# Optimization experiments

Measured on AMD Instinct MI355X. Metric: run time of the kernel, lower is better.

## Reference

```python
import jax, jax.numpy as jnp
import numpy as np

B, L = 4, 1024
D_MODEL, D_STATE, N_LAYERS, EXPAND = 512, 16, 4, 2
ED = EXPAND * D_MODEL            # 1024
DT_RANK = -(-D_MODEL // 16)       # ceil(d_model/16) = 32
D_CONV = 4
N_IN, N_OUT, N_FUT = 3, 2, 10
EPS = 1e-5


def setup_inputs() -> dict:
    key = jax.random.key(0)
    ks = jax.random.split(key, 16)
    s = 0.05
    inp = {
        "temporal_seq": jax.random.normal(ks[0], (B, L, N_IN), jnp.float32),
        # input / output projections (torch Linear: weight [out,in])
        "Wi": jax.random.normal(ks[1], (D_MODEL, N_IN), jnp.float32) * s,
        "bi": jnp.zeros((D_MODEL,), jnp.float32),
        "Wo": jax.random.normal(ks[2], (N_FUT * N_OUT, D_MODEL), jnp.float32) * s,
        "bo": jnp.zeros((N_FUT * N_OUT,), jnp.float32),
        # final LayerNorm
        "ln_g": jnp.ones((D_MODEL,), jnp.float32),
        "ln_b": jnp.zeros((D_MODEL,), jnp.float32),
        # stacked per-layer MambaBlock params
        "lWin": jax.random.normal(ks[3], (N_LAYERS, 2 * ED, D_MODEL), jnp.float32) * s,
        "lconvw": jax.random.normal(ks[4], (N_LAYERS, ED, 1, D_CONV), jnp.float32) * 0.2,
        "lconvb": jnp.zeros((N_LAYERS, ED), jnp.float32),
        "lWx": jax.random.normal(ks[5], (N_LAYERS, DT_RANK + 2 * D_STATE, ED), jnp.float32) * s,
        "lWdt": jax.random.normal(ks[6], (N_LAYERS, ED, DT_RANK), jnp.float32) * s,
        "lbdt": jnp.full((N_LAYERS, ED), -3.0, jnp.float32),  # small initial dt
        "lAlog": jnp.log(jnp.broadcast_to(jnp.arange(1.0, D_STATE + 1.0, dtype=jnp.float32), (N_LAYERS, ED, D_STATE))),
        "lD": jnp.ones((N_LAYERS, ED), jnp.float32),
        "lWout": jax.random.normal(ks[7], (N_LAYERS, D_MODEL, ED), jnp.float32) * s,
    }
    return inp


def _scan_op(l, r):
    al, bl = l
    ar, br = r
    return al * ar, ar * bl + br


def _mamba_block(x, Win, convw, convb, Wx, Wdt, bdt, Alog, Dp, Wout):
    # x: [B, L, D_MODEL]
    xz = jnp.einsum("bld,ed->ble", x, Win)          # [B, L, 2*ED]
    xb, z = jnp.split(xz, 2, axis=-1)
    # causal depthwise conv1d (padding d_conv-1 on the left == torch pad+trim)
    xc = jnp.transpose(xb, (0, 2, 1))                 # [B, ED, L]
    xc = jax.lax.conv_general_dilated(xc, convw, (1,), [(D_CONV - 1, 0)], feature_group_count=ED)
    xb = jnp.transpose(xc + convb[None, :, None], (0, 2, 1))
    xb = jax.nn.silu(xb)                              # [B, L, ED]
    # SSM parameters
    dbc = jnp.einsum("ble,fe->blf", xb, Wx)          # [B, L, DT_RANK+2N]
    delta = jax.nn.softplus(dbc[..., :DT_RANK] @ Wdt.T + bdt)   # [B, L, ED]
    Bm = dbc[..., DT_RANK:DT_RANK + D_STATE]          # [B, L, N]
    Cm = dbc[..., DT_RANK + D_STATE:]                 # [B, L, N]
    A = -jnp.exp(Alog)                                # [ED, N]
    dA = jnp.exp(delta[..., None] * A)                # [B, L, ED, N]
    dBx = (delta * xb)[..., None] * Bm[:, :, None, :] # [B, L, ED, N]
    # parallel associative scan: h_t = dA_t * h_{t-1} + dBx_t
    _, hs = jax.lax.associative_scan(_scan_op, (dA, dBx), axis=1)
    y = jnp.einsum("blen,bln->ble", hs, Cm) + Dp * xb
    y = y * jax.nn.silu(z)
    return jnp.einsum("ble,de->bld", y, Wout)


def reference(temporal_seq, Wi, bi, Wo, bo, ln_g, ln_b, lWin, lconvw, lconvb, lWx, lWdt, lbdt, lAlog, lD, lWout):
    x = temporal_seq @ Wi.T + bi                      # [B, L, D_MODEL]
    for i in range(N_LAYERS):
        x = _mamba_block(x, lWin[i], lconvw[i], lconvb[i], lWx[i], lWdt[i], lbdt[i], lAlog[i], lD[i], lWout[i])
    mu = jnp.mean(x, axis=-1, keepdims=True)
    var = jnp.mean((x - mu) ** 2, axis=-1, keepdims=True)
    x = (x - mu) / jnp.sqrt(var + EPS) * ln_g + ln_b
    h_final = x[:, -1, :]                             # [B, D_MODEL]
    u = h_final @ Wo.T + bo                           # [B, N_FUT*N_OUT]
    return u.reshape(-1, N_FUT, N_OUT)
```

## Files before the change

### kernel.cpp

```cpp
#include <hip/hip_runtime.h>
#include <hip/hip_bf16.h>
#include <math.h>

constexpr int Bx = 4, Lx = 1024, DM = 512, DS = 16, NL = 4, EDx = 1024;
constexpr int DTR = 32;

typedef __attribute__((ext_vector_type(8))) short short8v;
typedef __attribute__((ext_vector_type(4))) float f32x4;

__device__ inline short f2bf(float f) {
  union { __hip_bfloat16 h; short s; } u;
  u.h = __float2bfloat16(f);
  return u.s;
}
__device__ inline float bf2f(short s) {
  union { __hip_bfloat16 h; short s; } u;
  u.s = s;
  return __bfloat162float(u.h);
}

__global__ __launch_bounds__(256) void k_init_x(const float* __restrict__ seq,
    const float* __restrict__ Wi, const float* __restrict__ bi, float* __restrict__ x) {
  int idx = blockIdx.x * 256 + threadIdx.x;
  int d = idx & (DM - 1);
  int bl = idx >> 9;
  float s0 = seq[bl * 3 + 0], s1 = seq[bl * 3 + 1], s2 = seq[bl * 3 + 2];
  x[idx] = bi[d] + s0 * Wi[d * 3 + 0] + s1 * Wi[d * 3 + 1] + s2 * Wi[d * 3 + 2];
}

template <int BM, int BN>
__global__ __launch_bounds__(256) void k_gemm_mfma(
    const float* __restrict__ A, int lda,
    const float* __restrict__ W, int ldw,
    float* __restrict__ C, int ldc, int K) {
  constexpr int MR = BM / 32, NR = BN / 32;
  __shared__ short Ah[BM][44], Al[BM][44], Bh[BN][44], Bl[BN][44];
  const int tid = threadIdx.x;
  const int w = tid >> 6, lane = tid & 63;
  const int wr = w >> 1, wc = w & 1;
  const int r16 = lane & 15, kh = lane >> 4;
  const int m0 = blockIdx.x * BM, n0 = blockIdx.y * BN;

  f32x4 acc[MR][NR];
  #pragma unroll
  for (int i = 0; i < MR; ++i)
    #pragma unroll
    for (int j = 0; j < NR; ++j) {
      acc[i][j][0] = 0.f; acc[i][j][1] = 0.f; acc[i][j][2] = 0.f; acc[i][j][3] = 0.f;
    }

  for (int k0 = 0; k0 < K; k0 += 32) {
    __syncthreads();
    #pragma unroll
    for (int p = 0; p < BM / 32; ++p) {
      int f = tid + p * 256;
      int r = f >> 3, c = (f & 7) << 2;
      const float4 v = *(const float4*)(A + (size_t)(m0 + r) * lda + k0 + c);
      short h0 = f2bf(v.x), h1 = f2bf(v.y), h2 = f2bf(v.z), h3 = f2bf(v.w);
      Ah[r][c + 0] = h0; Ah[r][c + 1] = h1; Ah[r][c + 2] = h2; Ah[r][c + 3] = h3;
      Al[r][c + 0] = f2bf(v.x - bf2f(h0));
      Al[r][c + 1] = f2bf(v.y - bf2f(h1));
      Al[r][c + 2] = f2bf(v.z - bf2f(h2));
      Al[r][c + 3] = f2bf(v.w - bf2f(h3));
    }
    #pragma unroll
    for (int p = 0; p < BN / 32; ++p) {
      int f = tid + p * 256;
      int r = f >> 3, c = (f & 7) << 2;
      const float4 v = *(const float4*)(W + (size_t)(n0 + r) * ldw + k0 + c);
      short h0 = f2bf(v.x), h1 = f2bf(v.y), h2 = f2bf(v.z), h3 = f2bf(v.w);
      Bh[r][c + 0] = h0; Bh[r][c + 1] = h1; Bh[r][c + 2] = h2; Bh[r][c + 3] = h3;
      Bl[r][c + 0] = f2bf(v.x - bf2f(h0));
      Bl[r][c + 1] = f2bf(v.y - bf2f(h1));
      Bl[r][c + 2] = f2bf(v.z - bf2f(h2));
      Bl[r][c + 3] = f2bf(v.w - bf2f(h3));
    }
    __syncthreads();
    short8v ah[MR], al[MR], bh[NR], bl[NR];
    #pragma unroll
    for (int i = 0; i < MR; ++i) {
      int rr = wr * (BM / 2) + i * 16 + r16;
      ah[i] = *(const short8v*)(&Ah[rr][kh * 8]);
      al[i] = *(const short8v*)(&Al[rr][kh * 8]);
    }
    #pragma unroll
    for (int j = 0; j < NR; ++j) {
      int cc = wc * (BN / 2) + j * 16 + r16;
      bh[j] = *(const short8v*)(&Bh[cc][kh * 8]);
      bl[j] = *(const short8v*)(&Bl[cc][kh * 8]);
    }
    #pragma unroll
    for (int i = 0; i < MR; ++i)
      #pragma unroll
      for (int j = 0; j < NR; ++j) {
        acc[i][j] = __builtin_amdgcn_mfma_f32_16x16x32_bf16(ah[i], bh[j], acc[i][j], 0, 0, 0);
        acc[i][j] = __builtin_amdgcn_mfma_f32_16x16x32_bf16(ah[i], bl[j], acc[i][j], 0, 0, 0);
        acc[i][j] = __builtin_amdgcn_mfma_f32_16x16x32_bf16(al[i], bh[j], acc[i][j], 0, 0, 0);
      }
  }
  #pragma unroll
  for (int i = 0; i < MR; ++i) {
    int row_base = m0 + wr * (BM / 2) + i * 16 + kh * 4;
    #pragma unroll
    for (int j = 0; j < NR; ++j) {
      int col = n0 + wc * (BN / 2) + j * 16 + r16;
      #pragma unroll
      for (int r = 0; r < 4; ++r)
        C[(size_t)(row_base + r) * ldc + col] = acc[i][j][r];
    }
  }
}

template <int SK>
__global__ __launch_bounds__(256) void k_xproj_mfma(
    const float* __restrict__ A,
    const float* __restrict__ W,
    float* __restrict__ PART) {
  constexpr int BM = 128, BN = 64, KS = 1024 / SK;
  constexpr int MR = 4, NR = 2;
  __shared__ short Ah[BM][44], Al[BM][44], Bh[BN][44], Bl[BN][44];
  const int tid = threadIdx.x;
  const int w = tid >> 6, lane = tid & 63;
  const int wr = w >> 1, wc = w & 1;
  const int r16 = lane & 15, kh = lane >> 4;
  const int m0 = blockIdx.x * BM;
  const int kbeg = blockIdx.z * KS;

  f32x4 acc[MR][NR];
  #pragma unroll
  for (int i = 0; i < MR; ++i)
    #pragma unroll
    for (int j = 0; j < NR; ++j) {
      acc[i][j][0] = 0.f; acc[i][j][1] = 0.f; acc[i][j][2] = 0.f; acc[i][j][3] = 0.f;
    }

  for (int k0 = kbeg; k0 < kbeg + KS; k0 += 32) {
    __syncthreads();
    #pragma unroll
    for (int p = 0; p < BM / 32; ++p) {
      int f = tid + p * 256;
      int r = f >> 3, c = (f & 7) << 2;
      const float4 v = *(const float4*)(A + (size_t)(m0 + r) * 1024 + k0 + c);
      short h0 = f2bf(v.x), h1 = f2bf(v.y), h2 = f2bf(v.z), h3 = f2bf(v.w);
      Ah[r][c + 0] = h0; Ah[r][c + 1] = h1; Ah[r][c + 2] = h2; Ah[r][c + 3] = h3;
      Al[r][c + 0] = f2bf(v.x - bf2f(h0));
      Al[r][c + 1] = f2bf(v.y - bf2f(h1));
      Al[r][c + 2] = f2bf(v.z - bf2f(h2));
      Al[r][c + 3] = f2bf(v.w - bf2f(h3));
    }
    #pragma unroll
    for (int p = 0; p < BN / 32; ++p) {
      int f = tid + p * 256;
      int r = f >> 3, c = (f & 7) << 2;
      const float4 v = *(const float4*)(W + (size_t)r * 1024 + k0 + c);
      short h0 = f2bf(v.x), h1 = f2bf(v.y), h2 = f2bf(v.z), h3 = f2bf(v.w);
      Bh[r][c + 0] = h0; Bh[r][c + 1] = h1; Bh[r][c + 2] = h2; Bh[r][c + 3] = h3;
      Bl[r][c + 0] = f2bf(v.x - bf2f(h0));
      Bl[r][c + 1] = f2bf(v.y - bf2f(h1));
      Bl[r][c + 2] = f2bf(v.z - bf2f(h2));
      Bl[r][c + 3] = f2bf(v.w - bf2f(h3));
    }
    __syncthreads();
    short8v ah[MR], al[MR], bh[NR], bl[NR];
    #pragma unroll
    for (int i = 0; i < MR; ++i) {
      int rr = wr * 64 + i * 16 + r16;
      ah[i] = *(const short8v*)(&Ah[rr][kh * 8]);
      al[i] = *(const short8v*)(&Al[rr][kh * 8]);
    }
    #pragma unroll
    for (int j = 0; j < NR; ++j) {
      int cc = wc * 32 + j * 16 + r16;
      bh[j] = *(const short8v*)(&Bh[cc][kh * 8]);
      bl[j] = *(const short8v*)(&Bl[cc][kh * 8]);
    }
    #pragma unroll
    for (int i = 0; i < MR; ++i)
      #pragma unroll
      for (int j = 0; j < NR; ++j) {
        acc[i][j] = __builtin_amdgcn_mfma_f32_16x16x32_bf16(ah[i], bh[j], acc[i][j], 0, 0, 0);
        acc[i][j] = __builtin_amdgcn_mfma_f32_16x16x32_bf16(ah[i], bl[j], acc[i][j], 0, 0, 0);
        acc[i][j] = __builtin_amdgcn_mfma_f32_16x16x32_bf16(al[i], bh[j], acc[i][j], 0, 0, 0);
      }
  }
  float* Cp = PART + (size_t)blockIdx.z * (4096 * 64);
  #pragma unroll
  for (int i = 0; i < MR; ++i) {
    int row_base = m0 + wr * 64 + i * 16 + kh * 4;
    #pragma unroll
    for (int j = 0; j < NR; ++j) {
      int col = wc * 32 + j * 16 + r16;
      #pragma unroll
      for (int r = 0; r < 4; ++r)
        Cp[(size_t)(row_base + r) * 64 + col] = acc[i][j][r];
    }
  }
}

template <int SK>
__global__ __launch_bounds__(256) void k_redux(const float* __restrict__ PART,
                                               float* __restrict__ out) {
  int i = blockIdx.x * 256 + threadIdx.x;
  float4 s = ((const float4*)PART)[i];
  #pragma unroll
  for (int k = 1; k < SK; ++k) {
    const float4 v = ((const float4*)PART)[i + k * 65536];
    s.x += v.x; s.y += v.y; s.z += v.z; s.w += v.w;
  }
  ((float4*)out)[i] = s;
}

template <int BM, int BN, int EPI>
__global__ __launch_bounds__(256) void k_gemm_tn(
    const float* __restrict__ A, int lda,
    const float* __restrict__ W, int ldw,
    const float* __restrict__ bias,
    float* __restrict__ C, int ldc, int K) {
  constexpr int BK = 16;
  constexpr int MR = BM / 16, NR = BN / 16;
  __shared__ float As[BK][BM + 4];
  __shared__ float Bs[BK][BN + 4];
  const int tid = threadIdx.x;
  const int tx = tid & 15, ty = tid >> 4;
  const int m0 = blockIdx.x * BM, n0 = blockIdx.y * BN;
  const int arow = tid >> 2;
  const int akol = (tid & 3) << 2;
  float acc[MR][NR] = {};
  for (int k0 = 0; k0 < K; k0 += BK) {
    #pragma unroll
    for (int r = 0; r < BM / 64; ++r) {
      int m = arow + r * 64;
      const float4 v = *(const float4*)(A + (size_t)(m0 + m) * lda + k0 + akol);
      As[akol + 0][m] = v.x; As[akol + 1][m] = v.y;
      As[akol + 2][m] = v.z; As[akol + 3][m] = v.w;
    }
    if constexpr (BN >= 64) {
      #pragma unroll
      for (int r = 0; r < BN / 64; ++r) {
        int n = arow + r * 64;
        const float4 v = *(const float4*)(W + (size_t)(n0 + n) * ldw + k0 + akol);
        Bs[akol + 0][n] = v.x; Bs[akol + 1][n] = v.y;
        Bs[akol + 2][n] = v.z; Bs[akol + 3][n] = v.w;
      }
    } else {
      if (arow < BN) {
        const float4 v = *(const float4*)(W + (size_t)(n0 + arow) * ldw + k0 + akol);
        Bs[akol + 0][arow] = v.x; Bs[akol + 1][arow] = v.y;
        Bs[akol + 2][arow] = v.z; Bs[akol + 3][arow] = v.w;
      }
    }
    __syncthreads();
    #pragma unroll
    for (int k = 0; k < BK; ++k) {
      float af[MR], bf[NR];
      #pragma unroll
      for (int i = 0; i < MR; ++i) af[i] = As[k][ty * MR + i];
      #pragma unroll
      for (int j = 0; j < NR; ++j) bf[j] = Bs[k][tx * NR + j];
      #pragma unroll
      for (int i = 0; i < MR; ++i)
        #pragma unroll
        for (int j = 0; j < NR; ++j)
          acc[i][j] = fmaf(af[i], bf[j], acc[i][j]);
    }
    __syncthreads();
  }
  #pragma unroll
  for (int i = 0; i < MR; ++i) {
    int m = m0 + ty * MR + i;
    #pragma unroll
    for (int j = 0; j < NR; ++j) {
      int n = n0 + tx * NR + j;
      float v = acc[i][j];
      if constexpr (EPI == 1) {
        v += bias[n];
        v = (v > 20.f) ? v : log1pf(__expf(v));
      }
      C[(size_t)m * ldc + n] = v;
    }
  }
}

__global__ __launch_bounds__(256) void k_conv_silu(const float* __restrict__ xz,
    const float* __restrict__ cw, const float* __restrict__ cb, float* __restrict__ xb) {
  int idx = blockIdx.x * 256 + threadIdx.x;
  int e = idx & (EDx - 1);
  int bl = idx >> 10;
  int l = bl & (Lx - 1);
  const float4 w = ((const float4*)cw)[e];
  float acc = cb[e];
  if (l - 3 >= 0) acc = fmaf(xz[(size_t)(bl - 3) * (2 * EDx) + e], w.x, acc);
  if (l - 2 >= 0) acc = fmaf(xz[(size_t)(bl - 2) * (2 * EDx) + e], w.y, acc);
  if (l - 1 >= 0) acc = fmaf(xz[(size_t)(bl - 1) * (2 * EDx) + e], w.z, acc);
  acc = fmaf(xz[(size_t)bl * (2 * EDx) + e], w.w, acc);
  xb[idx] = acc / (1.f + __expf(-acc));
}

#define CVT4(V) { V.x = -__expf(V.x) * 1.44269504f; V.y = -__expf(V.y) * 1.44269504f; \
                  V.z = -__expf(V.z) * 1.44269504f; V.w = -__expf(V.w) * 1.44269504f; }

#define ST4PQ(Av, Pv, Qv, Bv) { \
  float a0 = exp2f(dl * Av.x); Pv.x *= a0; Qv.x = fmaf(a0, Qv.x, dx * Bv.x); \
  float a1 = exp2f(dl * Av.y); Pv.y *= a1; Qv.y = fmaf(a1, Qv.y, dx * Bv.y); \
  float a2 = exp2f(dl * Av.z); Pv.z *= a2; Qv.z = fmaf(a2, Qv.z, dx * Bv.z); \
  float a3 = exp2f(dl * Av.w); Pv.w *= a3; Qv.w = fmaf(a3, Qv.w, dx * Bv.w); }

#define ST4Y(Av, Hv, Bv, Cv) { \
  float a0 = exp2f(dl * Av.x); Hv.x = fmaf(a0, Hv.x, dx * Bv.x); y = fmaf(Hv.x, Cv.x, y); \
  float a1 = exp2f(dl * Av.y); Hv.y = fmaf(a1, Hv.y, dx * Bv.y); y = fmaf(Hv.y, Cv.y, y); \
  float a2 = exp2f(dl * Av.z); Hv.z = fmaf(a2, Hv.z, dx * Bv.z); y = fmaf(Hv.z, Cv.z, y); \
  float a3 = exp2f(dl * Av.w); Hv.w = fmaf(a3, Hv.w, dx * Bv.w); y = fmaf(Hv.w, Cv.w, y); }

template <int NCt>
__global__ __launch_bounds__(256) void k_scan1(
    const float* __restrict__ del, const float* __restrict__ xb,
    const float* __restrict__ dbc, const float* __restrict__ Alog,
    float* __restrict__ PQ) {
  constexpr int CTt = Lx / NCt;
  const int idx = blockIdx.x * 256 + threadIdx.x;
  const int ch = idx & 4095, c = idx >> 12;
  const int b = ch >> 10, e = ch & 1023;
  float4 A0, A1, A2, A3;
  {
    const float4* ar = (const float4*)(Alog + e * DS);
    A0 = ar[0]; A1 = ar[1]; A2 = ar[2]; A3 = ar[3];
    CVT4(A0); CVT4(A1); CVT4(A2); CVT4(A3);
  }
  float4 P0 = {1,1,1,1}, P1 = {1,1,1,1}, P2 = {1,1,1,1}, P3 = {1,1,1,1};
  float4 Q0 = {0,0,0,0}, Q1 = {0,0,0,0}, Q2 = {0,0,0,0}, Q3 = {0,0,0,0};
  const size_t bl0 = (size_t)b * Lx + c * CTt;
  const float* dp  = del + bl0 * EDx + e;
  const float* xp  = xb  + bl0 * EDx + e;
  const float* bcp = dbc + bl0 * 64 + 32;
  #pragma unroll 2
  for (int i = 0; i < CTt; ++i) {
    float dl = dp[0];
    float xbl = xp[0];
    float dx = dl * xbl;
    const float4* bp = (const float4*)bcp;
    float4 B0 = bp[0], B1 = bp[1], B2 = bp[2], B3 = bp[3];
    ST4PQ(A0, P0, Q0, B0); ST4PQ(A1, P1, Q1, B1);
    ST4PQ(A2, P2, Q2, B2); ST4PQ(A3, P3, Q3, B3);
    dp += EDx; xp += EDx; bcp += 64;
  }
  float4* o = (float4*)(PQ + (size_t)idx * 32);
  o[0] = P0; o[1] = P1; o[2] = P2; o[3] = P3;
  o[4] = Q0; o[5] = Q1; o[6] = Q2; o[7] = Q3;
}

template <int NCt>
__global__ __launch_bounds__(256) void k_scan2(float* __restrict__ PQ) {
  const int idx = blockIdx.x * 256 + threadIdx.x;
  const int ch = idx >> 4, n = idx & 15;
  constexpr int G = 8;
  const size_t off = (size_t)ch * 32 + n;
  float Pa[G], Qa[G], Pb[G], Qb[G];
  #pragma unroll
  for (int j = 0; j < G; ++j) {
    size_t base = (size_t)j * (4096 * 32) + off;
    Pa[j] = PQ[base]; Qa[j] = PQ[base + 16];
  }
  float H = 0.f;
  #pragma unroll
  for (int gp = 0; gp < NCt / (2 * G); ++gp) {
    const int cA = 2 * gp * G, cB = (2 * gp + 1) * G, cN = (2 * gp + 2) * G;
    #pragma unroll
    for (int j = 0; j < G; ++j) {
      size_t base = (size_t)(cB + j) * (4096 * 32) + off;
      Pb[j] = PQ[base]; Qb[j] = PQ[base + 16];
    }
    #pragma unroll
    for (int j = 0; j < G; ++j) {
      size_t base = (size_t)(cA + j) * (4096 * 32) + off;
      PQ[base + 16] = H;
      H = fmaf(Pa[j], H, Qa[j]);
    }
    if (gp + 1 < NCt / (2 * G)) {
      #pragma unroll
      for (int j = 0; j < G; ++j) {
        size_t base = (size_t)(cN + j) * (4096 * 32) + off;
        Pa[j] = PQ[base]; Qa[j] = PQ[base + 16];
      }
    }
    #pragma unroll
    for (int j = 0; j < G; ++j) {
      size_t base = (size_t)(cB + j) * (4096 * 32) + off;
      PQ[base + 16] = H;
      H = fmaf(Pb[j], H, Qb[j]);
    }
  }
}

template <int NCt>
__global__ __launch_bounds__(256) void k_scan3(
    float* __restrict__ dy,
    const float* __restrict__ xb,
    const float* __restrict__ dbc,
    const float* __restrict__ xz,
    const float* __restrict__ Alog, const float* __restrict__ Dp,
    const float* __restrict__ PQ) {
  constexpr int CTt = Lx / NCt;
  const int idx = blockIdx.x * 256 + threadIdx.x;
  const int ch = idx & 4095, c = idx >> 12;
  const int b = ch >> 10, e = ch & 1023;
  float4 A0, A1, A2, A3;
  {
    const float4* ar = (const float4*)(Alog + e * DS);
    A0 = ar[0]; A1 = ar[1]; A2 = ar[2]; A3 = ar[3];
    CVT4(A0); CVT4(A1); CVT4(A2); CVT4(A3);
  }
  float4 H0, H1, H2, H3;
  {
    const float4* hi = (const float4*)(PQ + (size_t)idx * 32 + 16);
    H0 = hi[0]; H1 = hi[1]; H2 = hi[2]; H3 = hi[3];
  }
  const float De = Dp[e];
  const size_t bl0 = (size_t)b * Lx + c * CTt;
  float* dyp = dy + bl0 * EDx + e;
  const float* xp  = xb + bl0 * EDx + e;
  const float* bcp = dbc + bl0 * 64 + 32;
  const float* zp  = xz + bl0 * (2 * EDx) + EDx + e;
  #pragma unroll 2
  for (int i = 0; i < CTt; ++i) {
    float dl = dyp[0];
    float xbl = xp[0];
    float zv = zp[0];
    float dx = dl * xbl;
    const float4* bp = (const float4*)bcp;
    float4 B0 = bp[0], B1 = bp[1], B2 = bp[2], B3 = bp[3];
    float4 C0 = bp[4], C1 = bp[5], C2 = bp[6], C3 = bp[7];
    float y = 0.f;
    ST4Y(A0, H0, B0, C0); ST4Y(A1, H1, B1, C1);
    ST4Y(A2, H2, B2, C2); ST4Y(A3, H3, B3, C3);
    y = fmaf(De, xbl, y);
    y *= zv / (1.f + __expf(-zv));
    dyp[0] = y;
    dyp += EDx; xp += EDx; bcp += 64; zp += 2 * EDx;
  }
}

__global__ __launch_bounds__(256) void k_ln_head(
    const float* __restrict__ x, const float* __restrict__ g,
    const float* __restrict__ be, const float* __restrict__ Wo,
    const float* __restrict__ bo, float* __restrict__ out) {
  const int b = blockIdx.x;
  const int t = threadIdx.x;
  const float* xr = x + ((size_t)b * Lx + (Lx - 1)) * DM;
  __shared__ float w1[4], w2[4];
  __shared__ float xn[DM];
  __shared__ float hp[20][8];
  float a0 = xr[t], a1 = xr[t + 256];
  float p = a0 + a1;
  #pragma unroll
  for (int o = 32; o > 0; o >>= 1) p += __shfl_down(p, o);
  if ((t & 63) == 0) w1[t >> 6] = p;
  __syncthreads();
  float mean = (w1[0] + w1[1] + w1[2] + w1[3]) * (1.f / DM);
  float d0 = a0 - mean, d1 = a1 - mean;
  p = d0 * d0 + d1 * d1;
  #pragma unroll
  for (int o = 32; o > 0; o >>= 1) p += __shfl_down(p, o);
  if ((t & 63) == 0) w2[t >> 6] = p;
  __syncthreads();
  float rstd = rsqrtf((w2[0] + w2[1] + w2[2] + w2[3]) * (1.f / DM) + 1e-5f);
  xn[t] = d0 * rstd * g[t] + be[t];
  xn[t + 256] = d1 * rstd * g[t + 256] + be[t + 256];
  __syncthreads();
  if (t < 160) {
    int j = t / 8, sg = t % 8;
    const float* wr = Wo + (size_t)j * DM + sg * 64;
    const float* xs = xn + sg * 64;
    float s = 0.f;
    #pragma unroll
    for (int k = 0; k < 64; ++k) s = fmaf(xs[k], wr[k], s);
    hp[j][sg] = s;
  }
  __syncthreads();
  if (t < 20) {
    float s = bo[t];
    #pragma unroll
    for (int k = 0; k < 8; ++k) s += hp[t][k];
    out[b * 20 + t] = s;
  }
}

extern "C" void kernel_launch(void* const* d_in, const int* in_sizes, int n_in,
                              void* d_out, int out_size, void* d_ws, size_t ws_size,
                              hipStream_t stream) {
  (void)in_sizes; (void)n_in; (void)out_size;
  const float* seq    = (const float*)d_in[0];
  const float* Wi     = (const float*)d_in[1];
  const float* bi     = (const float*)d_in[2];
  const float* Wo     = (const float*)d_in[3];
  const float* bo     = (const float*)d_in[4];
  const float* ln_g   = (const float*)d_in[5];
  const float* ln_b   = (const float*)d_in[6];
  const float* lWin   = (const float*)d_in[7];
  const float* lconvw = (const float*)d_in[8];
  const float* lconvb = (const float*)d_in[9];
  const float* lWx    = (const float*)d_in[10];
  const float* lWdt   = (const float*)d_in[11];
  const float* lbdt   = (const float*)d_in[12];
  const float* lAlog  = (const float*)d_in[13];
  const float* lD     = (const float*)d_in[14];
  const float* lWout  = (const float*)d_in[15];

  float* ws  = (float*)d_ws;
  float* X   = ws;
  float* XZ  = X + 2097152;
  float* XB  = XZ + 8388608;
  float* DBC = XB + 4194304;
  float* DEL = DBC + 262144;
  float* PQ  = DEL + 4194304;
  float* PART = PQ;

  const bool big = ws_size >= (size_t)110100480;

  k_init_x<<<dim3(Bx * Lx * DM / 256), 256, 0, stream>>>(seq, Wi, bi, X);

  for (int i = 0; i < NL; ++i) {
    const float* Win  = lWin   + (size_t)i * 2048 * 512;
    const float* cw   = lconvw + (size_t)i * EDx * 4;
    const float* cb   = lconvb + (size_t)i * EDx;
    const float* Wx   = lWx    + (size_t)i * 64 * EDx;
    const float* Wdt  = lWdt   + (size_t)i * EDx * DTR;
    const float* bdt  = lbdt   + (size_t)i * EDx;
    const float* Alog = lAlog  + (size_t)i * EDx * DS;
    const float* Dp   = lD     + (size_t)i * EDx;
    const float* Wout = lWout  + (size_t)i * DM * EDx;

    k_gemm_mfma<128, 128><<<dim3(32, 16), 256, 0, stream>>>(X, DM, Win, DM, XZ, 2 * EDx, DM);
    k_conv_silu<<<dim3(Bx * Lx * EDx / 256), 256, 0, stream>>>(XZ, cw, cb, XB);
    k_xproj_mfma<8><<<dim3(32, 1, 8), 256, 0, stream>>>(XB, Wx, PART);
    k_redux<8><<<dim3(256), 256, 0, stream>>>(PART, DBC);
    k_gemm_tn<128, 64, 1><<<dim3(32, 16), 256, 0, stream>>>(DBC, 64, Wdt, DTR, bdt, DEL, EDx, DTR);
    if (big) {
      k_scan1<64><<<dim3(4096 * 64 / 256), 256, 0, stream>>>(DEL, XB, DBC, Alog, PQ);
      k_scan2<64><<<dim3(4096 * DS / 256), 256, 0, stream>>>(PQ);
      k_scan3<64><<<dim3(4096 * 64 / 256), 256, 0, stream>>>(DEL, XB, DBC, XZ, Alog, Dp, PQ);
    } else {
      k_scan1<32><<<dim3(4096 * 32 / 256), 256, 0, stream>>>(DEL, XB, DBC, Alog, PQ);
      k_scan2<32><<<dim3(4096 * DS / 256), 256, 0, stream>>>(PQ);
      k_scan3<32><<<dim3(4096 * 32 / 256), 256, 0, stream>>>(DEL, XB, DBC, XZ, Alog, Dp, PQ);
    }
    k_gemm_mfma<128, 64><<<dim3(32, 8), 256, 0, stream>>>(DEL, EDx, Wout, EDx, X, DM, EDx);
  }

  k_ln_head<<<dim3(Bx), 256, 0, stream>>>(X, ln_g, ln_b, Wo, bo, (float*)d_out);
}
```

Before: 911.0 us.

## Pre-split GEMM operands into bf16 hi/lo buffers, vectorize conv, raise scan chunks

Adds a k_split kernel that converts fp32 activations and weights into separate bf16 hi/lo arrays before each GEMM. The GEMM then loads pre-split shorts directly instead of converting per tile, which removes repeated conversion work across blocks that reread the same rows. The depthwise conv+SiLU is vectorized to process four channels per thread with float4 loads. The scan chunk count moves from 64 to 128 when the workspace is large enough. The trade-off is extra kernel launches and extra global memory traffic for the split buffers, which are rebuilt every call, including for the weights.

```diff
diff --git a/kernel.cpp b/kernel.cpp
--- a/kernel.cpp
+++ b/kernel.cpp
@@ -6,6 +6,7 @@
 constexpr int DTR = 32;
 
 typedef __attribute__((ext_vector_type(8))) short short8v;
+typedef __attribute__((ext_vector_type(4))) short short4v;
 typedef __attribute__((ext_vector_type(4))) float f32x4;
 
 __device__ inline short f2bf(float f) {
@@ -17,6 +18,10 @@
   union { __hip_bfloat16 h; short s; } u;
   u.s = s;
   return __bfloat162float(u.h);
+}
+__device__ inline void store8(short* p, short8v v) {
+  *(short4v*)(p)     = __builtin_shufflevector(v, v, 0, 1, 2, 3);
+  *(short4v*)(p + 4) = __builtin_shufflevector(v, v, 4, 5, 6, 7);
 }
 
 __global__ __launch_bounds__(256) void k_init_x(const float* __restrict__ seq,
@@ -28,10 +33,23 @@
   x[idx] = bi[d] + s0 * Wi[d * 3 + 0] + s1 * Wi[d * 3 + 1] + s2 * Wi[d * 3 + 2];
 }
 
+__global__ __launch_bounds__(256) void k_split(const float* __restrict__ s,
+    short* __restrict__ hi, short* __restrict__ lo) {
+  int i = blockIdx.x * 256 + threadIdx.x;
+  const float4 v = ((const float4*)s)[i];
+  short4v h, l;
+  h.x = f2bf(v.x); l.x = f2bf(v.x - bf2f(h.x));
+  h.y = f2bf(v.y); l.y = f2bf(v.y - bf2f(h.y));
+  h.z = f2bf(v.z); l.z = f2bf(v.z - bf2f(h.z));
+  h.w = f2bf(v.w); l.w = f2bf(v.w - bf2f(h.w));
+  ((short4v*)hi)[i] = h;
+  ((short4v*)lo)[i] = l;
+}
+
 template <int BM, int BN>
-__global__ __launch_bounds__(256) void k_gemm_mfma(
-    const float* __restrict__ A, int lda,
-    const float* __restrict__ W, int ldw,
+__global__ __launch_bounds__(256) void k_gemm_bfp(
+    const short* __restrict__ Ahg, const short* __restrict__ Alg,
+    const short* __restrict__ Bhg, const short* __restrict__ Blg,
     float* __restrict__ C, int ldc, int K) {
   constexpr int MR = BM / 32, NR = BN / 32;
   __shared__ short Ah[BM][44], Al[BM][44], Bh[BN][44], Bl[BN][44];
@@ -52,28 +70,20 @@
   for (int k0 = 0; k0 < K; k0 += 32) {
     __syncthreads();
     #pragma unroll
-    for (int p = 0; p < BM / 32; ++p) {
+    for (int p = 0; p < BM / 64; ++p) {
       int f = tid + p * 256;
-      int r = f >> 3, c = (f & 7) << 2;
-      const float4 v = *(const float4*)(A + (size_t)(m0 + r) * lda + k0 + c);
-      short h0 = f2bf(v.x), h1 = f2bf(v.y), h2 = f2bf(v.z), h3 = f2bf(v.w);
-      Ah[r][c + 0] = h0; Ah[r][c + 1] = h1; Ah[r][c + 2] = h2; Ah[r][c + 3] = h3;
-      Al[r][c + 0] = f2bf(v.x - bf2f(h0));
-      Al[r][c + 1] = f2bf(v.y - bf2f(h1));
-      Al[r][c + 2] = f2bf(v.z - bf2f(h2));
-      Al[r][c + 3] = f2bf(v.w - bf2f(h3));
-    }
-    #pragma unroll
-    for (int p = 0; p < BN / 32; ++p) {
+      int r = f >> 2, c8 = (f & 3) << 3;
+      size_t g = (size_t)(m0 + r) * K + k0 + c8;
+      store8(&Ah[r][c8], *(const short8v*)(Ahg + g));
+      store8(&Al[r][c8], *(const short8v*)(Alg + g));
+    }
+    #pragma unroll
+    for (int p = 0; p < BN / 64; ++p) {
       int f = tid + p * 256;
-      int r = f >> 3, c = (f & 7) << 2;
-      const float4 v = *(const float4*)(W + (size_t)(n0 + r) * ldw + k0 + c);
-      short h0 = f2bf(v.x), h1 = f2bf(v.y), h2 = f2bf(v.z), h3 = f2bf(v.w);
-      Bh[r][c + 0] = h0; Bh[r][c + 1] = h1; Bh[r][c + 2] = h2; Bh[r][c + 3] = h3;
-      Bl[r][c + 0] = f2bf(v.x - bf2f(h0));
-      Bl[r][c + 1] = f2bf(v.y - bf2f(h1));
-      Bl[r][c + 2] = f2bf(v.z - bf2f(h2));
-      Bl[r][c + 3] = f2bf(v.w - bf2f(h3));
+      int r = f >> 2, c8 = (f & 3) << 3;
+      size_t g = (size_t)(n0 + r) * K + k0 + c8;
+      store8(&Bh[r][c8], *(const short8v*)(Bhg + g));
+      store8(&Bl[r][c8], *(const short8v*)(Blg + g));
     }
     __syncthreads();
     short8v ah[MR], al[MR], bh[NR], bl[NR];
@@ -281,19 +291,35 @@
   }
 }
 
-__global__ __launch_bounds__(256) void k_conv_silu(const float* __restrict__ xz,
+__global__ __launch_bounds__(256) void k_conv_silu4(const float* __restrict__ xz,
     const float* __restrict__ cw, const float* __restrict__ cb, float* __restrict__ xb) {
   int idx = blockIdx.x * 256 + threadIdx.x;
-  int e = idx & (EDx - 1);
-  int bl = idx >> 10;
+  int e4 = (idx & 255) << 2;
+  int bl = idx >> 8;
   int l = bl & (Lx - 1);
-  const float4 w = ((const float4*)cw)[e];
-  float acc = cb[e];
-  if (l - 3 >= 0) acc = fmaf(xz[(size_t)(bl - 3) * (2 * EDx) + e], w.x, acc);
-  if (l - 2 >= 0) acc = fmaf(xz[(size_t)(bl - 2) * (2 * EDx) + e], w.y, acc);
-  if (l - 1 >= 0) acc = fmaf(xz[(size_t)(bl - 1) * (2 * EDx) + e], w.z, acc);
-  acc = fmaf(xz[(size_t)bl * (2 * EDx) + e], w.w, acc);
-  xb[idx] = acc / (1.f + __expf(-acc));
+  const float4 w0 = ((const float4*)cw)[e4 + 0];
+  const float4 w1 = ((const float4*)cw)[e4 + 1];
+  const float4 w2 = ((const float4*)cw)[e4 + 2];
+  const float4 w3 = ((const float4*)cw)[e4 + 3];
+  float4 acc = ((const float4*)cb)[idx & 255];
+  const float* base = xz + (size_t)bl * (2 * EDx) + e4;
+  if (l >= 3) { const float4 x = *(const float4*)(base - 3 * 2 * EDx);
+    acc.x = fmaf(x.x, w0.x, acc.x); acc.y = fmaf(x.y, w1.x, acc.y);
+    acc.z = fmaf(x.z, w2.x, acc.z); acc.w = fmaf(x.w, w3.x, acc.w); }
+  if (l >= 2) { const float4 x = *(const float4*)(base - 2 * 2 * EDx);
+    acc.x = fmaf(x.x, w0.y, acc.x); acc.y = fmaf(x.y, w1.y, acc.y);
+    acc.z = fmaf(x.z, w2.y, acc.z); acc.w = fmaf(x.w, w3.y, acc.w); }
+  if (l >= 1) { const float4 x = *(const float4*)(base - 1 * 2 * EDx);
+    acc.x = fmaf(x.x, w0.z, acc.x); acc.y = fmaf(x.y, w1.z, acc.y);
+    acc.z = fmaf(x.z, w2.z, acc.z); acc.w = fmaf(x.w, w3.z, acc.w); }
+  { const float4 x = *(const float4*)(base);
+    acc.x = fmaf(x.x, w0.w, acc.x); acc.y = fmaf(x.y, w1.w, acc.y);
+    acc.z = fmaf(x.z, w2.w, acc.z); acc.w = fmaf(x.w, w3.w, acc.w); }
+  acc.x /= (1.f + __expf(-acc.x));
+  acc.y /= (1.f + __expf(-acc.y));
+  acc.z /= (1.f + __expf(-acc.z));
+  acc.w /= (1.f + __expf(-acc.w));
+  ((float4*)xb)[idx] = acc;
 }
 
 #define CVT4(V) { V.x = -__expf(V.x) * 1.44269504f; V.y = -__expf(V.y) * 1.44269504f; \
@@ -512,9 +538,19 @@
   float* DBC = XB + 4194304;
   float* DEL = DBC + 262144;
   float* PQ  = DEL + 4194304;
-  float* PART = PQ;
-
-  const bool big = ws_size >= (size_t)110100480;
+
+  short* PQs   = (short*)PQ;
+  short* Xh    = PQs;
+  short* Xl    = PQs + 2097152;
+  short* Winh  = PQs + 4194304;
+  short* Winl  = PQs + 5242880;
+  short* Yh    = PQs;
+  short* Yl    = PQs + 4194304;
+  short* Wouth = PQs + 8388608;
+  short* Woutl = PQs + 8912896;
+  float* PART  = PQ;
+
+  const bool nc128 = ws_size >= (size_t)143654912;
 
   k_init_x<<<dim3(Bx * Lx * DM / 256), 256, 0, stream>>>(seq, Wi, bi, X);
 
@@ -529,21 +565,25 @@
     const float* Dp   = lD     + (size_t)i * EDx;
     const float* Wout = lWout  + (size_t)i * DM * EDx;
 
-    k_gemm_mfma<128, 128><<<dim3(32, 16), 256, 0, stream>>>(X, DM, Win, DM, XZ, 2 * EDx, DM);
-    k_conv_silu<<<dim3(Bx * Lx * EDx / 256), 256, 0, stream>>>(XZ, cw, cb, XB);
+    k_split<<<dim3(2048), 256, 0, stream>>>(X, Xh, Xl);
+    k_split<<<dim3(1024), 256, 0, stream>>>(Win, Winh, Winl);
+    k_gemm_bfp<128, 128><<<dim3(32, 16), 256, 0, stream>>>(Xh, Xl, Winh, Winl, XZ, 2 * EDx, DM);
+    k_conv_silu4<<<dim3(Bx * Lx * EDx / 1024), 256, 0, stream>>>(XZ, cw, cb, XB);
     k_xproj_mfma<8><<<dim3(32, 1, 8), 256, 0, stream>>>(XB, Wx, PART);
     k_redux<8><<<dim3(256), 256, 0, stream>>>(PART, DBC);
     k_gemm_tn<128, 64, 1><<<dim3(32, 16), 256, 0, stream>>>(DBC, 64, Wdt, DTR, bdt, DEL, EDx, DTR);
-    if (big) {
+    if (nc128) {
+      k_scan1<128><<<dim3(4096 * 128 / 256), 256, 0, stream>>>(DEL, XB, DBC, Alog, PQ);
+      k_scan2<128><<<dim3(4096 * DS / 256), 256, 0, stream>>>(PQ);
+      k_scan3<128><<<dim3(4096 * 128 / 256), 256, 0, stream>>>(DEL, XB, DBC, XZ, Alog, Dp, PQ);
+    } else {
       k_scan1<64><<<dim3(4096 * 64 / 256), 256, 0, stream>>>(DEL, XB, DBC, Alog, PQ);
       k_scan2<64><<<dim3(4096 * DS / 256), 256, 0, stream>>>(PQ);
       k_scan3<64><<<dim3(4096 * 64 / 256), 256, 0, stream>>>(DEL, XB, DBC, XZ, Alog, Dp, PQ);
-    } else {
-      k_scan1<32><<<dim3(4096 * 32 / 256), 256, 0, stream>>>(DEL, XB, DBC, Alog, PQ);
-      k_scan2<32><<<dim3(4096 * DS / 256), 256, 0, stream>>>(PQ);
-      k_scan3<32><<<dim3(4096 * 32 / 256), 256, 0, stream>>>(DEL, XB, DBC, XZ, Alog, Dp, PQ);
-    }
-    k_gemm_mfma<128, 64><<<dim3(32, 8), 256, 0, stream>>>(DEL, EDx, Wout, EDx, X, DM, EDx);
+    }
+    k_split<<<dim3(4096), 256, 0, stream>>>(DEL, Yh, Yl);
+    k_split<<<dim3(512), 256, 0, stream>>>(Wout, Wouth, Woutl);
+    k_gemm_bfp<128, 64><<<dim3(32, 8), 256, 0, stream>>>(Yh, Yl, Wouth, Woutl, X, DM, EDx);
   }
 
   k_ln_head<<<dim3(Bx), 256, 0, stream>>>(X, ln_g, ln_b, Wo, bo, (float*)d_out);
```

After: 966.1 us. +6.0%, slower.

## Split scan state across thread pairs and vectorise conv-silu with float4

Applied to the files above, without the earlier changes.

The chunked scan kernels now give each (batch, channel, chunk) to two threads, each holding 8 of the 16 state dims. The pair combines its partial outputs with a lane shuffle and only one lane writes y. This doubles the thread count and halves per-thread registers, to raise occupancy and latency hiding in the scan. The cost is duplicated loads of delta, x and z per pair and an extra shuffle per step. The depthwise conv+SiLU kernel is also rewritten so each thread handles four channels with float4 loads and stores.

```diff
diff --git a/kernel.cpp b/kernel.cpp
--- a/kernel.cpp
+++ b/kernel.cpp
@@ -281,19 +281,35 @@
   }
 }
 
-__global__ __launch_bounds__(256) void k_conv_silu(const float* __restrict__ xz,
+__global__ __launch_bounds__(256) void k_conv_silu4(const float* __restrict__ xz,
     const float* __restrict__ cw, const float* __restrict__ cb, float* __restrict__ xb) {
   int idx = blockIdx.x * 256 + threadIdx.x;
-  int e = idx & (EDx - 1);
-  int bl = idx >> 10;
+  int e4 = (idx & 255) << 2;
+  int bl = idx >> 8;
   int l = bl & (Lx - 1);
-  const float4 w = ((const float4*)cw)[e];
-  float acc = cb[e];
-  if (l - 3 >= 0) acc = fmaf(xz[(size_t)(bl - 3) * (2 * EDx) + e], w.x, acc);
-  if (l - 2 >= 0) acc = fmaf(xz[(size_t)(bl - 2) * (2 * EDx) + e], w.y, acc);
-  if (l - 1 >= 0) acc = fmaf(xz[(size_t)(bl - 1) * (2 * EDx) + e], w.z, acc);
-  acc = fmaf(xz[(size_t)bl * (2 * EDx) + e], w.w, acc);
-  xb[idx] = acc / (1.f + __expf(-acc));
+  const float4 w0 = ((const float4*)cw)[e4 + 0];
+  const float4 w1 = ((const float4*)cw)[e4 + 1];
+  const float4 w2 = ((const float4*)cw)[e4 + 2];
+  const float4 w3 = ((const float4*)cw)[e4 + 3];
+  float4 acc = ((const float4*)cb)[idx & 255];
+  const float* base = xz + (size_t)bl * (2 * EDx) + e4;
+  if (l >= 3) { const float4 x = *(const float4*)(base - 3 * 2 * EDx);
+    acc.x = fmaf(x.x, w0.x, acc.x); acc.y = fmaf(x.y, w1.x, acc.y);
+    acc.z = fmaf(x.z, w2.x, acc.z); acc.w = fmaf(x.w, w3.x, acc.w); }
+  if (l >= 2) { const float4 x = *(const float4*)(base - 2 * 2 * EDx);
+    acc.x = fmaf(x.x, w0.y, acc.x); acc.y = fmaf(x.y, w1.y, acc.y);
+    acc.z = fmaf(x.z, w2.y, acc.z); acc.w = fmaf(x.w, w3.y, acc.w); }
+  if (l >= 1) { const float4 x = *(const float4*)(base - 1 * 2 * EDx);
+    acc.x = fmaf(x.x, w0.z, acc.x); acc.y = fmaf(x.y, w1.z, acc.y);
+    acc.z = fmaf(x.z, w2.z, acc.z); acc.w = fmaf(x.w, w3.z, acc.w); }
+  { const float4 x = *(const float4*)(base);
+    acc.x = fmaf(x.x, w0.w, acc.x); acc.y = fmaf(x.y, w1.w, acc.y);
+    acc.z = fmaf(x.z, w2.w, acc.z); acc.w = fmaf(x.w, w3.w, acc.w); }
+  acc.x /= (1.f + __expf(-acc.x));
+  acc.y /= (1.f + __expf(-acc.y));
+  acc.z /= (1.f + __expf(-acc.z));
+  acc.w /= (1.f + __expf(-acc.w));
+  ((float4*)xb)[idx] = acc;
 }
 
 #define CVT4(V) { V.x = -__expf(V.x) * 1.44269504f; V.y = -__expf(V.y) * 1.44269504f; \
@@ -318,34 +334,35 @@
     float* __restrict__ PQ) {
   constexpr int CTt = Lx / NCt;
   const int idx = blockIdx.x * 256 + threadIdx.x;
-  const int ch = idx & 4095, c = idx >> 12;
+  const int h8 = (idx & 1) << 3;
+  const int g = idx >> 1;
+  const int ch = g & 4095, c = g >> 12;
   const int b = ch >> 10, e = ch & 1023;
-  float4 A0, A1, A2, A3;
+  float4 A0, A1;
   {
-    const float4* ar = (const float4*)(Alog + e * DS);
-    A0 = ar[0]; A1 = ar[1]; A2 = ar[2]; A3 = ar[3];
-    CVT4(A0); CVT4(A1); CVT4(A2); CVT4(A3);
-  }
-  float4 P0 = {1,1,1,1}, P1 = {1,1,1,1}, P2 = {1,1,1,1}, P3 = {1,1,1,1};
-  float4 Q0 = {0,0,0,0}, Q1 = {0,0,0,0}, Q2 = {0,0,0,0}, Q3 = {0,0,0,0};
+    const float4* ar = (const float4*)(Alog + e * DS + h8);
+    A0 = ar[0]; A1 = ar[1];
+    CVT4(A0); CVT4(A1);
+  }
+  float4 P0 = {1,1,1,1}, P1 = {1,1,1,1};
+  float4 Q0 = {0,0,0,0}, Q1 = {0,0,0,0};
   const size_t bl0 = (size_t)b * Lx + c * CTt;
   const float* dp  = del + bl0 * EDx + e;
   const float* xp  = xb  + bl0 * EDx + e;
-  const float* bcp = dbc + bl0 * 64 + 32;
-  #pragma unroll 2
+  const float* bcp = dbc + bl0 * 64 + 32 + h8;
+  #pragma unroll 4
   for (int i = 0; i < CTt; ++i) {
     float dl = dp[0];
     float xbl = xp[0];
     float dx = dl * xbl;
     const float4* bp = (const float4*)bcp;
-    float4 B0 = bp[0], B1 = bp[1], B2 = bp[2], B3 = bp[3];
+    float4 B0 = bp[0], B1 = bp[1];
     ST4PQ(A0, P0, Q0, B0); ST4PQ(A1, P1, Q1, B1);
-    ST4PQ(A2, P2, Q2, B2); ST4PQ(A3, P3, Q3, B3);
     dp += EDx; xp += EDx; bcp += 64;
   }
-  float4* o = (float4*)(PQ + (size_t)idx * 32);
-  o[0] = P0; o[1] = P1; o[2] = P2; o[3] = P3;
-  o[4] = Q0; o[5] = Q1; o[6] = Q2; o[7] = Q3;
+  float4* o = (float4*)(PQ + (size_t)g * 32 + h8);
+  o[0] = P0; o[1] = P1;
+  o[4] = Q0; o[5] = Q1;
 }
 
 template <int NCt>
@@ -401,40 +418,43 @@
     const float* __restrict__ PQ) {
   constexpr int CTt = Lx / NCt;
   const int idx = blockIdx.x * 256 + threadIdx.x;
-  const int ch = idx & 4095, c = idx >> 12;
+  const int hh = idx & 1;
+  const int h8 = hh << 3;
+  const int g = idx >> 1;
+  const int ch = g & 4095, c = g >> 12;
   const int b = ch >> 10, e = ch & 1023;
-  float4 A0, A1, A2, A3;
+  float4 A0, A1;
   {
-    const float4* ar = (const float4*)(Alog + e * DS);
-    A0 = ar[0]; A1 = ar[1]; A2 = ar[2]; A3 = ar[3];
-    CVT4(A0); CVT4(A1); CVT4(A2); CVT4(A3);
-  }
-  float4 H0, H1, H2, H3;
+    const float4* ar = (const float4*)(Alog + e * DS + h8);
+    A0 = ar[0]; A1 = ar[1];
+    CVT4(A0); CVT4(A1);
+  }
+  float4 H0, H1;
   {
-    const float4* hi = (const float4*)(PQ + (size_t)idx * 32 + 16);
-    H0 = hi[0]; H1 = hi[1]; H2 = hi[2]; H3 = hi[3];
+    const float4* hi = (const float4*)(PQ + (size_t)g * 32 + 16 + h8);
+    H0 = hi[0]; H1 = hi[1];
   }
   const float De = Dp[e];
   const size_t bl0 = (size_t)b * Lx + c * CTt;
   float* dyp = dy + bl0 * EDx + e;
   const float* xp  = xb + bl0 * EDx + e;
-  const float* bcp = dbc + bl0 * 64 + 32;
+  const float* bcp = dbc + bl0 * 64 + 32 + h8;
   const float* zp  = xz + bl0 * (2 * EDx) + EDx + e;
-  #pragma unroll 2
+  #pragma unroll 4
   for (int i = 0; i < CTt; ++i) {
     float dl = dyp[0];
     float xbl = xp[0];
     float zv = zp[0];
     float dx = dl * xbl;
     const float4* bp = (const float4*)bcp;
-    float4 B0 = bp[0], B1 = bp[1], B2 = bp[2], B3 = bp[3];
-    float4 C0 = bp[4], C1 = bp[5], C2 = bp[6], C3 = bp[7];
+    float4 B0 = bp[0], B1 = bp[1];
+    float4 C0 = bp[4], C1 = bp[5];
     float y = 0.f;
     ST4Y(A0, H0, B0, C0); ST4Y(A1, H1, B1, C1);
-    ST4Y(A2, H2, B2, C2); ST4Y(A3, H3, B3, C3);
+    y += __shfl_xor(y, 1);
     y = fmaf(De, xbl, y);
     y *= zv / (1.f + __expf(-zv));
-    dyp[0] = y;
+    if (hh == 0) dyp[0] = y;
     dyp += EDx; xp += EDx; bcp += 64; zp += 2 * EDx;
   }
 }
@@ -514,7 +534,7 @@
   float* PQ  = DEL + 4194304;
   float* PART = PQ;
 
-  const bool big = ws_size >= (size_t)110100480;
+  const bool nc64 = ws_size >= (size_t)110100480;
 
   k_init_x<<<dim3(Bx * Lx * DM / 256), 256, 0, stream>>>(seq, Wi, bi, X);
 
@@ -530,18 +550,18 @@
     const float* Wout = lWout  + (size_t)i * DM * EDx;
 
     k_gemm_mfma<128, 128><<<dim3(32, 16), 256, 0, stream>>>(X, DM, Win, DM, XZ, 2 * EDx, DM);
-    k_conv_silu<<<dim3(Bx * Lx * EDx / 256), 256, 0, stream>>>(XZ, cw, cb, XB);
+    k_conv_silu4<<<dim3(Bx * Lx * EDx / 1024), 256, 0, stream>>>(XZ, cw, cb, XB);
     k_xproj_mfma<8><<<dim3(32, 1, 8), 256, 0, stream>>>(XB, Wx, PART);
     k_redux<8><<<dim3(256), 256, 0, stream>>>(PART, DBC);
     k_gemm_tn<128, 64, 1><<<dim3(32, 16), 256, 0, stream>>>(DBC, 64, Wdt, DTR, bdt, DEL, EDx, DTR);
-    if (big) {
-      k_scan1<64><<<dim3(4096 * 64 / 256), 256, 0, stream>>>(DEL, XB, DBC, Alog, PQ);
+    if (nc64) {
+      k_scan1<64><<<dim3(64 * 32), 256, 0, stream>>>(DEL, XB, DBC, Alog, PQ);
       k_scan2<64><<<dim3(4096 * DS / 256), 256, 0, stream>>>(PQ);
-      k_scan3<64><<<dim3(4096 * 64 / 256), 256, 0, stream>>>(DEL, XB, DBC, XZ, Alog, Dp, PQ);
+      k_scan3<64><<<dim3(64 * 32), 256, 0, stream>>>(DEL, XB, DBC, XZ, Alog, Dp, PQ);
     } else {
-      k_scan1<32><<<dim3(4096 * 32 / 256), 256, 0, stream>>>(DEL, XB, DBC, Alog, PQ);
+      k_scan1<32><<<dim3(32 * 32), 256, 0, stream>>>(DEL, XB, DBC, Alog, PQ);
       k_scan2<32><<<dim3(4096 * DS / 256), 256, 0, stream>>>(PQ);
-      k_scan3<32><<<dim3(4096 * 32 / 256), 256, 0, stream>>>(DEL, XB, DBC, XZ, Alog, Dp, PQ);
+      k_scan3<32><<<dim3(32 * 32), 256, 0, stream>>>(DEL, XB, DBC, XZ, Alog, Dp, PQ);
     }
     k_gemm_mfma<128, 64><<<dim3(32, 8), 256, 0, stream>>>(DEL, EDx, Wout, EDx, X, DM, EDx);
   }
```

Measured after the change: 842.2 us. -7.5%, faster.
